# Performance work log

Hardware: AMD Instinct MI355X
Metric: run time of the kernel (lower is better)

The kernel has to match this reference:

```python
import jax, jax.numpy as jnp
import numpy as np

JIT = 1e-4
LOG2PI = float(np.log(2.0 * np.pi))
BETA = 1e5
LOC_RADIUS = 5.0


def gaspari_cohn(radius, D):
    i = np.arange(D)
    dist = np.minimum(np.abs(i[:, None] - i[None, :]), D - np.abs(i[:, None] - i[None, :])).astype(np.float64)
    z = dist / radius
    zs = np.maximum(z, 1e-12)
    g1 = 1.0 - 5.0 / 3 * z**2 + 5.0 / 8 * z**3 + 0.5 * z**4 - 0.25 * z**5
    g2 = 4.0 - 5.0 * z + 5.0 / 3 * z**2 + 5.0 / 8 * z**3 - 0.5 * z**4 + 1.0 / 12 * z**5 - 2.0 / (3.0 * zs)
    return np.where(z < 1.0, g1, np.where(z < 2.0, g2, 0.0)).astype(np.float32)


def sq_dist(x, z):
    # x: [..., n, d], z: [..., m, d] (broadcastable)
    x2 = jnp.sum(x * x, -1)[..., :, None]
    z2 = jnp.sum(z * z, -1)[..., None, :]
    d2 = x2 + z2 - 2.0 * jnp.matmul(x, jnp.swapaxes(z, -1, -2))
    return jnp.maximum(d2, 0.0)


def setup_inputs():
    key = jax.random.key(0)
    ks = jax.random.split(key, 12)
    D, dy, M, N, B, T = 32, 32, 128, 128, 8, 48
    ips = jax.random.normal(ks[0], (D, M, D), dtype=jnp.float32)
    H = jnp.eye(dy, D, dtype=jnp.float32)
    lengthscale = jnp.full((D,), 2.0, dtype=jnp.float32)
    outputscale = jnp.ones((D,), dtype=jnp.float32)
    q_mu = 0.1 * jax.random.normal(ks[1], (D, M), dtype=jnp.float32)
    q_L = jnp.tril(0.02 * jax.random.normal(ks[2], (D, M, M), dtype=jnp.float32), -1) + 0.1 * jnp.eye(M, dtype=jnp.float32)[None]
    q_noise = jnp.full((D,), 0.05**2, dtype=jnp.float32)
    r_noise = jnp.full((dy,), 0.1**2, dtype=jnp.float32)
    x0 = jax.random.normal(ks[3], (N, D, B, D), dtype=jnp.float32)
    y = 0.5 * jax.random.normal(ks[4], (B, T, dy), dtype=jnp.float32)
    eps_u = jax.random.normal(ks[5], (N, D, M), dtype=jnp.float32)
    eps_f = jax.random.normal(ks[6], (T, N, D, B), dtype=jnp.float32)
    eps_q = jax.random.normal(ks[7], (T, B, N, D), dtype=jnp.float32)
    eps_r = jax.random.normal(ks[8], (T, B, N, dy), dtype=jnp.float32)
    return {"ips": ips, "H": H, "lengthscale": lengthscale, "outputscale": outputscale,
            "q_mu": q_mu, "q_L": q_L, "q_noise": q_noise, "r_noise": r_noise,
            "x0": x0, "y": y, "eps_u": eps_u, "eps_f": eps_f, "eps_q": eps_q, "eps_r": eps_r}


def _forward(ips, H, lengthscale, outputscale, q_mu, q_L, q_noise, r_noise, x0, y, eps_u, eps_f, eps_q, eps_r):
    N, D, B, _ = x0.shape
    M = ips.shape[1]
    dy = y.shape[-1]
    taper = jnp.asarray(gaspari_cohn(LOC_RADIUS, D))
    ls = lengthscale[:, None, None]
    osc = outputscale[:, None, None]
    zs = ips / ls  # [D, M, D]
    Kzz = osc * jnp.exp(-0.5 * sq_dist(zs, zs)) + JIT * jnp.eye(M, dtype=x0.dtype)  # [D,M,M]
    # U ~ q(u): consistent sampling of inducing outputs per ensemble member
    U = q_mu[None] + jnp.einsum('dmk,ndk->ndm', q_L, eps_u)                 # [N,D,M]
    A = jnp.linalg.solve(Kzz[None], U[..., None])[..., 0]                    # Kzz^{-1} u, [N,D,M]
    # KL(q(u) || N(0, Kzz)) summed over tasks
    Lzz = jnp.linalg.cholesky(Kzz)
    Sq = q_L @ jnp.swapaxes(q_L, -1, -2)
    trace = jnp.sum(jnp.diagonal(jnp.linalg.solve(Kzz, Sq), axis1=-2, axis2=-1))
    mah = jnp.sum(q_mu * jnp.linalg.solve(Kzz, q_mu[..., None])[..., 0])
    logdetK = 2.0 * jnp.sum(jnp.log(jnp.diagonal(Lzz, axis1=-2, axis2=-1)))
    logdetS = 2.0 * jnp.sum(jnp.log(jnp.abs(jnp.diagonal(q_L, axis1=-2, axis2=-1))))
    kl = 0.5 * (trace + mah - D * M + logdetK - logdetS)

    q_sd = jnp.sqrt(q_noise)
    r_sd = jnp.sqrt(r_noise)
    R = jnp.diag(r_noise)
    Ht = H.T
    eyeB = jnp.eye(B, dtype=x0.dtype)

    def step(carry, inp):
        x_prev, ll = carry
        y_t, ef, eq, er = inp
        # ---- GP prediction (conditioned on sampled U) ----
        xq = x_prev / lengthscale[None, :, None, None]                       # [N,D,B,D]
        Kxz = outputscale[None, :, None, None] * jnp.exp(-0.5 * sq_dist(xq, zs[None]))  # [N,D,B,M]
        Kxx = outputscale[None, :, None, None] * jnp.exp(-0.5 * sq_dist(xq, xq))        # [N,D,B,B]
        mean = jnp.einsum('ndbm,ndm->ndb', Kxz, A)
        V = jnp.linalg.solve(Kzz[None], jnp.swapaxes(Kxz, -1, -2))           # [N,D,M,B]
        cov = Kxx - jnp.matmul(Kxz, V) + JIT * eyeB
        Lc = jnp.linalg.cholesky(cov)
        f = mean + jnp.einsum('ndbc,ndc->ndb', Lc, ef)                       # rsample, [N,D,B]
        X = jnp.transpose(f, (2, 0, 1))                                      # [B,N,D]
        X = X + eq * q_sd                                                    # + chol(Q) noise
        Xm = jnp.mean(X, axis=-2, keepdims=True)                             # [B,1,D]
        Xc = X - Xm
        P = taper * (jnp.swapaxes(Xc, -1, -2) @ Xc) / (N - 1)                # localized cov [B,D,D]
        # ---- EnKF update ----
        S = H @ P @ Ht + R                                                   # [B,dy,dy]
        Ls = jnp.linalg.cholesky(S)
        resid = y_t - (Xm @ Ht)[:, 0]                                        # [B,dy]
        alpha = jnp.linalg.solve(S, resid[..., None])[..., 0]
        logdetS_t = 2.0 * jnp.sum(jnp.log(jnp.diagonal(Ls, axis1=-2, axis2=-1)), axis=-1)
        ll_t = -0.5 * jnp.sum(dy * LOG2PI + logdetS_t + jnp.sum(resid * alpha, -1))
        PHt = P @ Ht
        K = jnp.swapaxes(jnp.linalg.solve(S, jnp.swapaxes(PHt, -1, -2)), -1, -2)  # [B,D,dy]
        y_pert = y_t[:, None, :] + er * r_sd
        X_post = X + (y_pert - X @ Ht) @ jnp.swapaxes(K, -1, -2)
        Xm_post = jnp.mean(X_post, axis=-2)                                  # [B,D]
        P_post = P - K @ (H @ P)
        x_next = jnp.broadcast_to(Xm_post[None, None], (N, D, B, D))         # ensemble reset to post. mean
        return (x_next, ll + ll_t), (Xm_post, jnp.diagonal(P_post, axis1=-2, axis2=-1))

    ys = jnp.swapaxes(y, 0, 1)  # [T,B,dy]
    (x_final, ll), (fm, fv) = jax.lax.scan(step, (x0, jnp.asarray(0.0, x0.dtype)), (ys, eps_f, eps_q, eps_r))
    filtered_mean = jnp.swapaxes(fm, 0, 1)  # [B,T,D]
    filtered_var = jnp.swapaxes(fv, 0, 1)   # [B,T,D]
    elbo = ll - kl / BETA
    return elbo, x_final, filtered_mean, filtered_var


def reference(ips, H, lengthscale, outputscale, q_mu, q_L, q_noise, r_noise, x0, y, eps_u, eps_f, eps_q, eps_r):
    return _forward(ips, H, lengthscale, outputscale, q_mu, q_L, q_noise, r_noise, x0, y, eps_u, eps_f, eps_q, eps_r)
```

## Files before the change

### kernel.cpp

```cpp
#include <hip/hip_runtime.h>

#define JITF 1e-4f
#define LOG2PIF 1.8378770664093454f

#define WZSM   0
#define WZS2   131072
#define WKINV  135168
#define WA     659456
#define WU     1183744
#define WXW    1708032
#define WXM    1740800
#define WLLB   1741056
#define WKLD   1741088
#define WCNT   1741248
#define OFM 1048577
#define OFV 1060865

__device__ __forceinline__ float dot4f(const float4 a, const float4 b) {
  return fmaf(a.x, b.x, fmaf(a.y, b.y, fmaf(a.z, b.z, a.w * b.w)));
}
__device__ __forceinline__ float4 f4_fma(const float4 a, const float s, const float4 c) {
  return make_float4(fmaf(a.x,s,c.x), fmaf(a.y,s,c.y), fmaf(a.z,s,c.z), fmaf(a.w,s,c.w));
}
__device__ __forceinline__ float4 f4_axpby(const float a, const float4 x, const float b, const float4 y) {
  return make_float4(fmaf(a,x.x,b*y.x), fmaf(a,x.y,b*y.y), fmaf(a,x.z,b*y.z), fmaf(a,x.w,b*y.w));
}
__device__ __forceinline__ float aloadf(const float* p) {
  return __hip_atomic_load((float*)p, __ATOMIC_RELAXED, __HIP_MEMORY_SCOPE_AGENT);
}
__device__ __forceinline__ void astoref(float* p, float v) {
  __hip_atomic_store(p, v, __ATOMIC_RELAXED, __HIP_MEMORY_SCOPE_AGENT);
}
__device__ __forceinline__ unsigned long long aloadu(const unsigned long long* p) {
  return __hip_atomic_load((unsigned long long*)p, __ATOMIC_RELAXED, __HIP_MEMORY_SCOPE_AGENT);
}
__device__ __forceinline__ void pollge(const int* p, int target) {
  while (__hip_atomic_load((int*)p, __ATOMIC_RELAXED, __HIP_MEMORY_SCOPE_AGENT) < target)
    __builtin_amdgcn_s_sleep(1);
}
__device__ __forceinline__ void gsignal(int* p, int val, int tid) {
  __syncthreads();
  if (tid == 0) __hip_atomic_store(p, val, __ATOMIC_RELEASE, __HIP_MEMORY_SCOPE_AGENT);
}

__global__ __launch_bounds__(512) void k_sweep(
    const float* __restrict__ ips, const float* __restrict__ ls, const float* __restrict__ osc,
    const float* __restrict__ qL, const float* __restrict__ qmu,
    float* __restrict__ zsMg, float* __restrict__ zs2g,
    float* __restrict__ Kinvg, float* __restrict__ kld, int* cnt)
{
  __shared__ float sm[22792];
  float* cur   = sm;
  float* zsM   = sm + 16896;
  float* rowP0 = sm + 21504;
  float* rowP1 = sm + 21636;
  float* colP0 = sm + 21768;
  float* colP1 = sm + 21896;
  float* qms   = sm + 22024;
  float* zs2   = sm + 22152;
  float* red   = sm + 22280;
  float4* cur4 = (float4*)cur;
  const float4* zsM4 = (const float4*)zsM;
  float4* rowP04 = (float4*)rowP0;
  float4* rowP14 = (float4*)rowP1;
  const int d = blockIdx.x, tid = threadIdx.x;
  const float invl = 1.0f / ls[d], oscd = osc[d];

  if (blockIdx.x == 0) { for (int l = tid; l < 640; l += 512) cnt[l] = 0; }

  for (int l = tid; l < 4096; l += 512) {
    int m = l >> 5, k = l & 31;
    zsM[m*36+k] = ips[(d*128+m)*32+k] * invl;
  }
  if (tid < 128) qms[tid] = qmu[d*128+tid];
  __syncthreads();
  if (tid < 128) {
    float s = 0.f;
#pragma unroll
    for (int kq = 0; kq < 8; kq++) { float4 v = zsM4[tid*9+kq]; s += dot4f(v, v); }
    zs2[tid] = s; zs2g[d*128+tid] = s;
  }
  for (int l = tid; l < 4096; l += 512) zsMg[d*4096+l] = zsM[(l>>5)*36 + (l&31)];
  __syncthreads();

  const int i = tid >> 2, q = tid & 3;
  {
    float4 zr[8];
#pragma unroll
    for (int kq = 0; kq < 8; kq++) zr[kq] = zsM4[i*9+kq];
    float z2i = zs2[i];
    for (int jj = 0; jj < 32; jj++) {
      int j = q*32 + jj;
      float dot = 0.f;
#pragma unroll
      for (int kq = 0; kq < 8; kq++) dot += dot4f(zr[kq], zsM4[j*9+kq]);
      float d2 = fmaxf(z2i + zs2[j] - 2.f*dot, 0.f);
      cur[i*132+j] = oscd * expf(-0.5f*d2) + (i == j ? JITF : 0.f);
    }
  }
  __syncthreads();

  float llog = 0.f;
#pragma unroll 1
  for (int kb = 0; kb < 64; kb++) {
    const int k0 = 2*kb, k1 = k0+1;
    if (tid < 33) rowP04[tid] = cur4[k0*33 + tid];
    else if (tid < 66) rowP14[tid-33] = cur4[k1*33 + (tid-33)];
    else if (tid < 194) colP0[tid-66] = cur[(tid-66)*132 + k0];
    else if (tid < 322) colP1[tid-194] = cur[(tid-194)*132 + k1];
    __syncthreads();
    const float a  = rowP0[k0];
    const float bb = rowP0[k1];
    const float c  = rowP1[k1];
    const float det = fmaf(a, c, -bb*bb);
    const float idet = 1.0f/det;
    if (tid == 0) llog += logf(det);
    const float ci0 = colP0[i], ci1 = colP1[i];
    const float w0 = (ci0*c - ci1*bb)*idet;
    const float w1 = (ci1*a - ci0*bb)*idet;
    const bool isk0 = (i == k0), isk1 = (i == k1);
    const int jqp = k0 >> 2;
    const int c0 = k0 & 3;
#pragma unroll
    for (int jj = 0; jj < 8; jj++) {
      int jq = q*8 + jj;
      float4 r0 = rowP04[jq];
      float4 r1 = rowP14[jq];
      float4 nv;
      if (isk0)      nv = f4_axpby(c*idet, r0, -bb*idet, r1);
      else if (isk1) nv = f4_axpby(-bb*idet, r0, a*idet, r1);
      else {
        nv = cur4[i*33+jq];
        nv = f4_fma(r0, -w0, nv);
        nv = f4_fma(r1, -w1, nv);
      }
      if (jq == jqp) {
        float pv0, pv1;
        if (isk0)      { pv0 = -c*idet;  pv1 =  bb*idet; }
        else if (isk1) { pv0 =  bb*idet; pv1 = -a*idet;  }
        else           { pv0 =  w0;      pv1 =  w1;      }
        if (c0 == 0) { nv.x = pv0; nv.y = pv1; }
        else         { nv.z = pv0; nv.w = pv1; }
      }
      cur4[i*33+jq] = nv;
    }
    __syncthreads();
  }
  for (int e = tid; e < 16384; e += 512) { int ii = e>>7, jj = e&127; cur[ii*132+jj] = -cur[ii*132+jj]; }
  __syncthreads();
  for (int l = tid; l < 4096; l += 512) ((float4*)(Kinvg + d*16384))[l] = cur4[(l>>5)*33 + (l&31)];

  if (tid == 0) kld[d] = 0.5f * llog;
  red[tid] = (tid < 128) ? logf(fabsf(qL[(d*128+tid)*128+tid])) : 0.f;
  __syncthreads();
  for (int s = 256; s > 0; s >>= 1) { if (tid < s) red[tid] += red[tid+s]; __syncthreads(); }
  if (tid == 0) kld[96+d] = red[0];
  __syncthreads();
  {
    float macc = 0.f;
    for (int e = tid; e < 16384; e += 512) {
      int ii = e >> 7, jj = e & 127;
      macc = fmaf(cur[ii*132+jj], qms[ii]*qms[jj], macc);
    }
    red[tid] = macc;
    __syncthreads();
    for (int s = 256; s > 0; s >>= 1) { if (tid < s) red[tid] += red[tid+s]; __syncthreads(); }
    if (tid == 0) kld[64+d] = red[0];
    __syncthreads();
  }
  {
    float tacc = 0.f;
    for (int e = tid; e < 16384; e += 512) {
      int ii = e >> 7, k2 = e & 127;
      if (k2 <= ii) {
        float w = 0.f;
        for (int m = k2; m < 128; m++) w = fmaf(cur[ii*132+m], qL[(d*128+m)*128+k2], w);
        tacc = fmaf(w, qL[(d*128+ii)*128+k2], tacc);
      }
    }
    red[tid] = tacc;
    __syncthreads();
    for (int s = 256; s > 0; s >>= 1) { if (tid < s) red[tid] += red[tid+s]; __syncthreads(); }
    if (tid == 0) kld[32+d] = red[0];
  }
}

__global__ __launch_bounds__(128) void k_U(
    const float* __restrict__ qL, const float* __restrict__ qmu, const float* __restrict__ eu,
    float* __restrict__ U)
{
  __shared__ float qLs[128][129];
  __shared__ float eus[128];
  const int d = blockIdx.x >> 2, nc = blockIdx.x & 3, tid = threadIdx.x;
  for (int l = tid; l < 16384; l += 128) qLs[l >> 7][l & 127] = qL[d * 16384 + l];
  __syncthreads();
  const float qm = qmu[d * 128 + tid];
  for (int nn = 0; nn < 32; nn++) {
    int n = nc * 32 + nn;
    eus[tid] = eu[(n * 32 + d) * 128 + tid];
    __syncthreads();
    int kmax = tid + 1;
    int k4 = kmax & ~3;
    float s0 = qm, s1 = 0.f, s2 = 0.f, s3 = 0.f;
    int k = 0;
    for (; k < k4; k += 4) {
      s0 = fmaf(qLs[tid][k], eus[k], s0);
      s1 = fmaf(qLs[tid][k + 1], eus[k + 1], s1);
      s2 = fmaf(qLs[tid][k + 2], eus[k + 2], s2);
      s3 = fmaf(qLs[tid][k + 3], eus[k + 3], s3);
    }
    for (; k < kmax; k++) s0 = fmaf(qLs[tid][k], eus[k], s0);
    U[(n * 32 + d) * 128 + tid] = (s0 + s1) + (s2 + s3);
    __syncthreads();
  }
}

__global__ __launch_bounds__(256) void k_A2(
    const float* __restrict__ Kinv, const float* __restrict__ U, float* __restrict__ A)
{
  __shared__ float Kis[128][129];
  __shared__ float Us[32][129];
  const int d = blockIdx.x >> 2, nc = blockIdx.x & 3, tid = threadIdx.x;
  const int n0 = nc * 32;
  for (int l = tid; l < 16384; l += 256) Kis[l >> 7][l & 127] = Kinv[d * 16384 + l];
  for (int l = tid; l < 4096; l += 256) Us[l >> 7][l & 127] = U[((n0 + (l >> 7)) * 32 + d) * 128 + (l & 127)];
  __syncthreads();
  for (int e = tid; e < 4096; e += 256) {
    int nl = e >> 7, m = e & 127;
    float s0 = 0.f, s1 = 0.f, s2 = 0.f, s3 = 0.f;
    for (int k = 0; k < 128; k += 4) {
      s0 = fmaf(Kis[m][k], Us[nl][k], s0);
      s1 = fmaf(Kis[m][k + 1], Us[nl][k + 1], s1);
      s2 = fmaf(Kis[m][k + 2], Us[nl][k + 2], s2);
      s3 = fmaf(Kis[m][k + 3], Us[nl][k + 3], s3);
    }
    A[((n0 + nl) * 32 + d) * 128 + m] = (s0 + s1) + (s2 + s3);
  }
}

__global__ __launch_bounds__(128) void k_t0gp(
    const float* __restrict__ x0, const float* __restrict__ ls, const float* __restrict__ osc,
    const float* __restrict__ qn, const float* __restrict__ zsMg, const float* __restrict__ zs2g,
    const float* __restrict__ Kinv, const float* __restrict__ A,
    const float* __restrict__ ef, const float* __restrict__ eq, float* __restrict__ Xw)
{
  __shared__ float xqs[8*36];
  __shared__ float xq2s[8];
  __shared__ float Kxzs[8*132];
  __shared__ float T1s[8*132];
  __shared__ float covs[8][9];
  __shared__ float Lc[8][9];
  __shared__ float Arow[132];
  const float4* xqs4  = (const float4*)xqs;
  const float4* Kxzs4 = (const float4*)Kxzs;
  const float4* T1s4  = (const float4*)T1s;
  const float4* Arow4 = (const float4*)Arow;
  const int n = blockIdx.x >> 5, d = blockIdx.x & 31, tid = threadIdx.x;
  const float invl = 1.0f / ls[d], oscd = osc[d];

  float4 zr[8];
  {
    const float4* zrow = (const float4*)(zsMg + d*4096 + tid*32);
#pragma unroll
    for (int kq = 0; kq < 8; kq++) zr[kq] = zrow[kq];
  }
  const float z2m = zs2g[d*128 + tid];
  for (int l = tid; l < 256; l += 128) {
    int b = l >> 5, k = l & 31;
    xqs[b*36+k] = x0[((n*32+d)*8 + b)*32 + k] * invl;
  }
  Arow[tid] = A[(n*32+d)*128 + tid];
  __syncthreads();
  if (tid < 8) {
    float s = 0.f;
#pragma unroll
    for (int kq = 0; kq < 8; kq++) { float4 v = xqs4[tid*9+kq]; s += dot4f(v, v); }
    xq2s[tid] = s;
  }
  __syncthreads();
  {
#pragma unroll
    for (int b = 0; b < 8; b++) {
      float dot = 0.f;
#pragma unroll
      for (int kq = 0; kq < 8; kq++) dot += dot4f(zr[kq], xqs4[b*9+kq]);
      Kxzs[b*132+tid] = oscd * expf(-0.5f * fmaxf(xq2s[b] + z2m - 2.f*dot, 0.f));
    }
  }
  __syncthreads();
  {
    float a[8] = {0.f,0.f,0.f,0.f,0.f,0.f,0.f,0.f};
    const float* kp = Kinv + d*16384 + tid;
    for (int mq = 0; mq < 32; mq++) {
      float kv0 = kp[(4*mq+0)*128];
      float kv1 = kp[(4*mq+1)*128];
      float kv2 = kp[(4*mq+2)*128];
      float kv3 = kp[(4*mq+3)*128];
#pragma unroll
      for (int b = 0; b < 8; b++) {
        float4 kx = Kxzs4[b*33+mq];
        a[b] = fmaf(kx.x, kv0, fmaf(kx.y, kv1, fmaf(kx.z, kv2, fmaf(kx.w, kv3, a[b]))));
      }
    }
#pragma unroll
    for (int b = 0; b < 8; b++) T1s[b*132+tid] = a[b];
  }
  __syncthreads();
  if (tid < 64) {
    int b = tid >> 3, c = tid & 7;
    float sc = 0.f, dt = 0.f;
#pragma unroll
    for (int mq = 0; mq < 32; mq++) sc += dot4f(T1s4[b*33+mq], Kxzs4[c*33+mq]);
#pragma unroll
    for (int kq = 0; kq < 8; kq++) dt += dot4f(xqs4[b*9+kq], xqs4[c*9+kq]);
    float kxx = oscd * expf(-0.5f * fmaxf(xq2s[b] + xq2s[c] - 2.f*dt, 0.f));
    covs[b][c] = kxx - sc + (b == c ? JITF : 0.f);
  }
  __syncthreads();
  if (tid == 0) {
    for (int a = 0; a < 8; a++) {
      float s = covs[a][a];
      for (int k = 0; k < a; k++) s -= Lc[a][k]*Lc[a][k];
      float la = sqrtf(s);
      Lc[a][a] = la;
      for (int i2 = a+1; i2 < 8; i2++) {
        float s2 = covs[i2][a];
        for (int k = 0; k < a; k++) s2 -= Lc[i2][k]*Lc[a][k];
        Lc[i2][a] = s2 / la;
      }
    }
  }
  __syncthreads();
  if (tid < 8) {
    int b = tid;
    float mv = 0.f;
#pragma unroll
    for (int mq = 0; mq < 32; mq++) mv += dot4f(Kxzs4[b*33+mq], Arow4[mq]);
    float f = mv;
#pragma unroll
    for (int c = 0; c < 8; c++) if (c <= b) f = fmaf(Lc[b][c], ef[(n*32+d)*8 + c], f);
    float X = f + eq[(b*128+n)*32 + d] * sqrtf(qn[d]);
    Xw[(d*8+b)*128 + n] = X;
  }
}

__global__ __launch_bounds__(1024) void k_scan(
    const float* __restrict__ ls, const float* __restrict__ osc,
    const float* __restrict__ qn, const float* __restrict__ rn,
    const float* __restrict__ y,
    const float* __restrict__ ef, const float* __restrict__ eq, const float* __restrict__ er,
    const float* __restrict__ zsMg, const float* __restrict__ zs2g,
    const float* __restrict__ Kinvg, const float* __restrict__ Ag,
    float* Xw, float* xm, float* llb, const float* __restrict__ kld,
    float* out, int* cnt)
{
  __shared__ float sm[36704];
  const int blk = blockIdx.x, tid = threadIdx.x;

  if (blk < 32) {
    const int d = blk;
    float* KinvS = sm;
    float* AT    = sm + 16512;
    float* KxzS  = sm + 33024;
    float* T1S   = sm + 34080;
    float* xqS   = sm + 35136;
    float* efS   = sm + 35424;
    float* covS  = sm + 36576;
    const float invl = 1.0f/ls[d], oscd = osc[d], qsd = sqrtf(qn[d]);
    const float4* KxzS4 = (const float4*)KxzS;
    const float4* T1S4  = (const float4*)T1S;
    const float4* xqS4  = (const float4*)xqS;
    const unsigned long long* xm_u = (const unsigned long long*)xm;

    for (int l = tid; l < 16384; l += 1024)
      KinvS[(l>>7)*129 + (l&127)] = Kinvg[d*16384 + l];
    for (int l = tid; l < 16384; l += 1024) {
      int n = l >> 7, m = l & 127;
      AT[m*129 + n] = Ag[(n*32 + d)*128 + m];
    }

    const int bb = tid >> 7, mn = tid & 127;
    float4 zr[8];
    {
      const float4* zrow = (const float4*)(zsMg + d*4096 + mn*32);
#pragma unroll
      for (int kq = 0; kq < 8; kq++) zr[kq] = zrow[kq];
    }
    const float z2m = zs2g[d*128 + mn];
    __syncthreads();

    for (int t = 1; t < 48; t++) {
      const float v_ef = ef[((t*128 + (tid>>3))*32 + d)*8 + (tid&7)];
      const float v_eq = eq[((t*8+bb)*128 + mn)*32 + d];

      if (tid < 8) pollge(cnt + (32+tid)*16, t);
      __syncthreads();
      if (tid < 128) {
        unsigned long long u = aloadu(xm_u + tid);
        float2 f = __builtin_bit_cast(float2, u);
        int b2 = tid >> 4, k2 = (tid & 15)*2;
        xqS[b2*36 + k2]     = f.x * invl;
        xqS[b2*36 + k2 + 1] = f.y * invl;
      }
      efS[(tid>>3)*9 + (tid&7)] = v_ef;
      __syncthreads();
      {
        float dot = 0.f, sq = 0.f;
#pragma unroll
        for (int kq = 0; kq < 8; kq++) {
          float4 x4 = xqS4[bb*9+kq];
          dot += dot4f(zr[kq], x4);
          sq  += dot4f(x4, x4);
        }
        KxzS[bb*132+mn] = oscd * expf(-0.5f * fmaxf(sq + z2m - 2.f*dot, 0.f));
      }
      __syncthreads();
      float mv;
      {
        float t1a = 0.f, t1b = 0.f, ma = 0.f, mb2 = 0.f;
#pragma unroll 8
        for (int mm = 0; mm < 128; mm += 2) {
          float kx0 = KxzS[bb*132+mm], kx1 = KxzS[bb*132+mm+1];
          t1a = fmaf(kx0, KinvS[mm*129+mn],     t1a);
          t1b = fmaf(kx1, KinvS[(mm+1)*129+mn], t1b);
          ma  = fmaf(kx0, AT[mm*129+mn],        ma);
          mb2 = fmaf(kx1, AT[(mm+1)*129+mn],    mb2);
        }
        T1S[bb*132+mn] = t1a + t1b;
        mv = ma + mb2;
      }
      __syncthreads();
      if (tid < 64) {
        int b = tid >> 3, c = tid & 7;
        float sc = 0.f, dt = 0.f, sqb = 0.f, sqc = 0.f;
#pragma unroll
        for (int mq = 0; mq < 32; mq++) sc += dot4f(T1S4[b*33+mq], KxzS4[c*33+mq]);
#pragma unroll
        for (int kq = 0; kq < 8; kq++) {
          float4 xb = xqS4[b*9+kq], xc = xqS4[c*9+kq];
          dt += dot4f(xb, xc); sqb += dot4f(xb, xb); sqc += dot4f(xc, xc);
        }
        float kxx = oscd*expf(-0.5f*fmaxf(sqb + sqc - 2.f*dt, 0.f));
        covS[b*9+c] = kxx - sc + (b==c ? JITF : 0.f);
      }
      __syncthreads();
      {
        float Lc[8][8];
        float f = mv;
#pragma unroll
        for (int a = 0; a < 8; a++) {
          float s = covS[a*9+a];
#pragma unroll
          for (int k = 0; k < 8; k++) if (k < a) s -= Lc[a][k]*Lc[a][k];
          float la = sqrtf(s);
          Lc[a][a] = la;
          if (a == bb) f = fmaf(la, efS[mn*9+a], f);
          float ila = 1.0f / la;
#pragma unroll
          for (int i2 = 0; i2 < 8; i2++) if (i2 > a) {
            float s2 = covS[i2*9+a];
#pragma unroll
            for (int k = 0; k < 8; k++) if (k < a) s2 -= Lc[i2][k]*Lc[a][k];
            float lv = s2 * ila;
            Lc[i2][a] = lv;
            if (i2 == bb) f = fmaf(lv, efS[mn*9+a], f);
          }
        }
        f = fmaf(v_eq, qsd, f);
        astoref(Xw + (d*8+bb)*128 + mn, f);
      }
      gsignal(cnt + d*16, t, tid);
    }
    if (tid < 8) pollge(cnt + (32+tid)*16, 48);
    __syncthreads();
  } else {
    const int b = blk - 32;
    float* XN     = sm;
    float* Ps     = sm + 4224;
    float* Sinvs  = sm + 5376;
    float* taperS = sm + 6432;
    float* mersS  = sm + 7456;
    float* rowP   = sm + 8992;
    float* colP   = sm + 9136;
    float* detS   = sm + 9280;
    float* XmsS   = sm + 9296;
    float* residS = sm + 9328;
    float* miS    = sm + 9360;
    float* rsdS   = sm + 9392;
    float* rnS    = sm + 9424;
    const float4* er4 = (const float4*)er;
    const unsigned long long* Xw_u = (const unsigned long long*)Xw;

    if (tid < 1024) {
      int ii = tid >> 5, jj = tid & 31;
      int ad = ii - jj; if (ad < 0) ad = -ad;
      int dist = (ad < 32 - ad) ? ad : (32 - ad);
      double z = (double)dist / 5.0;
      double z2 = z*z, z3 = z2*z, z4 = z3*z, z5 = z4*z;
      double gval;
      if (z < 1.0) gval = 1.0 - (5.0/3.0)*z2 + (5.0/8.0)*z3 + 0.5*z4 - 0.25*z5;
      else if (z < 2.0) gval = 4.0 - 5.0*z + (5.0/3.0)*z2 + (5.0/8.0)*z3 - 0.5*z4 + (1.0/12.0)*z5 - 2.0/(3.0*z);
      else gval = 0.0;
      taperS[tid] = (float)gval;
    }
    if (tid < 32) { rnS[tid] = rn[tid]; rsdS[tid] = sqrtf(rn[tid]); }
    if (tid < 384) {
      int tt = tid >> 3, jq = tid & 7;
      float sx = 0.f, sy = 0.f, sz = 0.f, sw = 0.f;
      for (int n = 0; n < 128; n++) {
        float4 e = er4[((tt*8+b)*128+n)*8 + jq];
        sx += e.x; sy += e.y; sz += e.z; sw += e.w;
      }
      int o = tt*32 + jq*4;
      mersS[o]   = sx*(1.f/128.f);
      mersS[o+1] = sy*(1.f/128.f);
      mersS[o+2] = sz*(1.f/128.f);
      mersS[o+3] = sw*(1.f/128.f);
    }
    __syncthreads();

    float llacc = 0.f;
    const int i = tid >> 5, j = tid & 31;
    for (int t = 0; t < 48; t++) {
      float yv = 0.f;
      if (tid < 32) yv = y[(b*48+t)*32 + tid];
      if (t > 0) { if (tid < 32) pollge(cnt + tid*16, t); }
      __syncthreads();
      {
        unsigned long long u0 = aloadu(Xw_u + (i*8+b)*64 + j);
        unsigned long long u1 = aloadu(Xw_u + (i*8+b)*64 + j + 32);
        float2 f0 = __builtin_bit_cast(float2, u0);
        float2 f1 = __builtin_bit_cast(float2, u1);
        float s4 = (f0.x+f0.y)+(f1.x+f1.y);
#pragma unroll
        for (int mk = 1; mk <= 16; mk <<= 1) s4 += __shfl_xor(s4, mk, 64);
        float mu = s4 * (1.f/128.f);
        if (j == 0) XmsS[i] = mu;
        XN[(2*j)*33+i]    = f0.x - mu;
        XN[(2*j+1)*33+i]  = f0.y - mu;
        XN[(2*j+64)*33+i] = f1.x - mu;
        XN[(2*j+65)*33+i] = f1.y - mu;
      }
      __syncthreads();
      float val;
      {
        float a0 = 0.f, a1 = 0.f;
#pragma unroll 4
        for (int n = 0; n < 128; n += 2) {
          a0 = fmaf(XN[n*33+i],     XN[n*33+j],     a0);
          a1 = fmaf(XN[(n+1)*33+i], XN[(n+1)*33+j], a1);
        }
        float pv = taperS[i*32+j] * (a0+a1) * (1.f/127.f);
        Ps[i*36+j] = pv;
        val = pv + ((i==j) ? rnS[i] : 0.f);
      }
#pragma unroll 1
      for (int kb = 0; kb < 16; kb++) {
        int k0 = kb*2, k1 = k0+1, par = (kb&1)*72;
        if (i == k0) rowP[par + j]      = val;
        if (i == k1) rowP[par + 36 + j] = val;
        if (j == k0) colP[par + i]      = val;
        if (j == k1) colP[par + 36 + i] = val;
        __syncthreads();
        float a  = rowP[par + k0];
        float bb = rowP[par + k1];
        float c  = rowP[par + 36 + k1];
        float det = fmaf(a, c, -bb*bb);
        float idet = 1.0f/det;
        float ci0 = colP[par + i], ci1 = colP[par + 36 + i];
        float r0j = rowP[par + j], r1j = rowP[par + 36 + j];
        float w0 = (ci0*c - ci1*bb)*idet;
        float w1 = (ci1*a - ci0*bb)*idet;
        float v0 = (c*r0j - bb*r1j)*idet;
        float v1 = (a*r1j - bb*r0j)*idet;
        float nv = val - w0*r0j - w1*r1j;
        if (i == k0) nv = v0;
        if (i == k1) nv = v1;
        if (j == k0) nv = w0;
        if (j == k1) nv = w1;
        if (i == k0 && j == k0) nv = -c*idet;
        if (i == k0 && j == k1) nv =  bb*idet;
        if (i == k1 && j == k0) nv =  bb*idet;
        if (i == k1 && j == k1) nv = -a*idet;
        val = nv;
        if (tid == 0) detS[kb] = det;
      }
      Sinvs[i*33+j] = -val;
      if (tid < 32) {
        float rs = yv - XmsS[tid];
        residS[tid] = rs;
        miS[tid] = fmaf(mersS[t*32+tid], rsdS[tid], rs);
      }
      __syncthreads();
      if (tid < 32) {
        float bt = 0.f;
#pragma unroll
        for (int k = 0; k < 32; k++) bt = fmaf(Sinvs[tid*33+k], miS[k], bt);
        float xmp = XmsS[tid] + miS[tid] - rnS[tid]*bt;
        out[OFM + (b*48+t)*32 + tid] = xmp;
        out[OFV + (b*48+t)*32 + tid] = rnS[tid] - rnS[tid]*rnS[tid]*Sinvs[tid*33+tid];
        astoref(xm + b*32 + tid, xmp);
      } else if (tid < 64) {
        int ii = tid - 32;
        float al = 0.f;
#pragma unroll
        for (int k = 0; k < 32; k++) al = fmaf(Sinvs[ii*33+k], residS[k], al);
        float contrib = al * residS[ii] + ((ii < 16) ? logf(detS[ii]) : 0.f);
#pragma unroll
        for (int mk = 1; mk <= 16; mk <<= 1) contrib += __shfl_xor(contrib, mk, 64);
        if (ii == 0) {
          llacc += -0.5f*(32.f*LOG2PIF + contrib);
          if (t == 47) astoref(llb + b, llacc);
        }
      }
      gsignal(cnt + (32+b)*16, t+1, tid);
    }
    if (tid < 8) pollge(cnt + (32+tid)*16, 48);
    __syncthreads();
  }

  if (tid < 128) {
    unsigned long long u = aloadu((const unsigned long long*)xm + tid);
    float2 f = __builtin_bit_cast(float2, u);
    sm[2*tid] = f.x; sm[2*tid+1] = f.y;
  }
  __syncthreads();
  for (int v = blk*1024 + tid; v < 1048576; v += 40960)
    out[1 + v] = sm[v & 255];
  if (blk == 32 && tid == 0) {
    double ll = 0.0;
    for (int i2 = 0; i2 < 8; i2++) ll += (double)aloadf(llb + i2);
    double ldK = 0.0, tr = 0.0, mah = 0.0, ldS = 0.0;
    for (int d2 = 0; d2 < 32; d2++) {
      ldK += (double)kld[d2];
      tr  += (double)kld[32+d2];
      mah += (double)kld[64+d2];
      ldS += (double)kld[96+d2];
    }
    double klv = 0.5*(tr + mah - 4096.0 + 2.0*ldK - 2.0*ldS);
    out[0] = (float)(ll - klv/100000.0);
  }
}

extern "C" void kernel_launch(void* const* d_in, const int* in_sizes, int n_in,
                              void* d_out, int out_size, void* d_ws, size_t ws_size,
                              hipStream_t stream) {
  const float* ips = (const float*)d_in[0];
  const float* ls  = (const float*)d_in[2];
  const float* osc = (const float*)d_in[3];
  const float* qmu = (const float*)d_in[4];
  const float* qL  = (const float*)d_in[5];
  const float* qn  = (const float*)d_in[6];
  const float* rn  = (const float*)d_in[7];
  const float* x0  = (const float*)d_in[8];
  const float* y   = (const float*)d_in[9];
  const float* eu  = (const float*)d_in[10];
  const float* ef  = (const float*)d_in[11];
  const float* eq  = (const float*)d_in[12];
  const float* er  = (const float*)d_in[13];
  float* out = (float*)d_out;
  float* ws  = (float*)d_ws;

  float* w_zsm  = ws + WZSM;
  float* w_zs2  = ws + WZS2;
  float* w_kinv = ws + WKINV;
  float* w_A    = ws + WA;
  float* w_U    = ws + WU;
  float* w_Xw   = ws + WXW;
  float* w_xm   = ws + WXM;
  float* w_llb  = ws + WLLB;
  float* w_kld  = ws + WKLD;
  int*   w_cnt  = (int*)(ws + WCNT);

  k_sweep<<<32, 512, 0, stream>>>(ips, ls, osc, qL, qmu, w_zsm, w_zs2, w_kinv, w_kld, w_cnt);
  k_U<<<128, 128, 0, stream>>>(qL, qmu, eu, w_U);
  k_A2<<<128, 256, 0, stream>>>(w_kinv, w_U, w_A);
  k_t0gp<<<4096, 128, 0, stream>>>(x0, ls, osc, qn, w_zsm, w_zs2, w_kinv, w_A, ef, eq, w_Xw);
  void* args[] = { (void*)&ls, (void*)&osc, (void*)&qn, (void*)&rn, (void*)&y,
                   (void*)&ef, (void*)&eq, (void*)&er, (void*)&w_zsm, (void*)&w_zs2,
                   (void*)&w_kinv, (void*)&w_A, (void*)&w_Xw, (void*)&w_xm, (void*)&w_llb,
                   (void*)&w_kld, (void*)&out, (void*)&w_cnt };
  hipLaunchCooperativeKernel((void*)k_scan, dim3(40), dim3(1024), args, 0, stream);
}
```

Measured before the change: 1.917 ms.

## Register-block GP mean/T1 matvec, symmetric covariance, and 4x4-block Gauss-Jordan inverse

In the per-dimension blocks, the Kxz·Kinv and Kxz·A products are now computed by 256 threads. Each thread holds float4 rows of Kinv/A and reuses them across 4 batch rows. Results are written to shared memory instead of each of 1024 threads doing a scalar dot. In the filter blocks, the ensemble covariance uses only the 528 upper-triangle entries via float4 dot products and a mean correction instead of explicit centering. The in-place inversion now pivots on 4x4 blocks, which halves the number of barrier-separated steps. The changes aim to cut LDS traffic and sync count on the serial scan path, at the cost of fewer active threads, more registers, and possible cancellation in the uncentered covariance.

```diff
diff --git a/kernel.cpp b/kernel.cpp
--- a/kernel.cpp
+++ b/kernel.cpp
@@ -354,29 +354,32 @@
     float* Xw, float* xm, float* llb, const float* __restrict__ kld,
     float* out, int* cnt)
 {
-  __shared__ float sm[36704];
+  __shared__ float sm[38740];
   const int blk = blockIdx.x, tid = threadIdx.x;
 
   if (blk < 32) {
     const int d = blk;
     float* KinvS = sm;
-    float* AT    = sm + 16512;
-    float* KxzS  = sm + 33024;
-    float* T1S   = sm + 34080;
-    float* xqS   = sm + 35136;
-    float* efS   = sm + 35424;
-    float* covS  = sm + 36576;
+    float* AS    = sm + 16896;
+    float* KxzS  = sm + 33792;
+    float* T1S   = sm + 34848;
+    float* MeanS = sm + 35904;
+    float* xqS   = sm + 36960;
+    float* efS   = sm + 37248;
+    float* covS  = sm + 38400;
     const float invl = 1.0f/ls[d], oscd = osc[d], qsd = sqrtf(qn[d]);
-    const float4* KxzS4 = (const float4*)KxzS;
-    const float4* T1S4  = (const float4*)T1S;
-    const float4* xqS4  = (const float4*)xqS;
+    const float4* KinvS4 = (const float4*)KinvS;
+    const float4* AS4    = (const float4*)AS;
+    const float4* KxzS4  = (const float4*)KxzS;
+    const float4* T1S4   = (const float4*)T1S;
+    const float4* xqS4   = (const float4*)xqS;
     const unsigned long long* xm_u = (const unsigned long long*)xm;
 
     for (int l = tid; l < 16384; l += 1024)
-      KinvS[(l>>7)*129 + (l&127)] = Kinvg[d*16384 + l];
+      KinvS[(l>>7)*132 + (l&127)] = Kinvg[d*16384 + l];
     for (int l = tid; l < 16384; l += 1024) {
       int n = l >> 7, m = l & 127;
-      AT[m*129 + n] = Ag[(n*32 + d)*128 + m];
+      AS[n*132 + m] = Ag[(n*32 + d)*128 + m];
     }
 
     const int bb = tid >> 7, mn = tid & 127;
@@ -415,19 +418,26 @@
         KxzS[bb*132+mn] = oscd * expf(-0.5f * fmaxf(sq + z2m - 2.f*dot, 0.f));
       }
       __syncthreads();
-      float mv;
-      {
-        float t1a = 0.f, t1b = 0.f, ma = 0.f, mb2 = 0.f;
+      if (tid < 256) {
+        const int bq = tid >> 7, mq = tid & 127;
+        float t1a[4] = {0.f,0.f,0.f,0.f};
+        float mea[4] = {0.f,0.f,0.f,0.f};
 #pragma unroll 8
-        for (int mm = 0; mm < 128; mm += 2) {
-          float kx0 = KxzS[bb*132+mm], kx1 = KxzS[bb*132+mm+1];
-          t1a = fmaf(kx0, KinvS[mm*129+mn],     t1a);
-          t1b = fmaf(kx1, KinvS[(mm+1)*129+mn], t1b);
-          ma  = fmaf(kx0, AT[mm*129+mn],        ma);
-          mb2 = fmaf(kx1, AT[(mm+1)*129+mn],    mb2);
+        for (int mmq = 0; mmq < 32; mmq++) {
+          float4 kv = KinvS4[mq*33 + mmq];
+          float4 av = AS4[mq*33 + mmq];
+#pragma unroll
+          for (int c = 0; c < 4; c++) {
+            float4 kx = KxzS4[(bq + 2*c)*33 + mmq];
+            t1a[c] += dot4f(kx, kv);
+            mea[c] += dot4f(kx, av);
+          }
         }
-        T1S[bb*132+mn] = t1a + t1b;
-        mv = ma + mb2;
+#pragma unroll
+        for (int c = 0; c < 4; c++) {
+          T1S[(bq + 2*c)*132 + mq]   = t1a[c];
+          MeanS[(bq + 2*c)*132 + mq] = mea[c];
+        }
       }
       __syncthreads();
       if (tid < 64) {
@@ -446,7 +456,7 @@
       __syncthreads();
       {
         float Lc[8][8];
-        float f = mv;
+        float f = MeanS[bb*132 + mn];
 #pragma unroll
         for (int a = 0; a < 8; a++) {
           float s = covS[a*9+a];
@@ -475,19 +485,20 @@
     __syncthreads();
   } else {
     const int b = blk - 32;
-    float* XN     = sm;
+    float* XT     = sm;
     float* Ps     = sm + 4224;
     float* Sinvs  = sm + 5376;
     float* taperS = sm + 6432;
     float* mersS  = sm + 7456;
     float* rowP   = sm + 8992;
-    float* colP   = sm + 9136;
-    float* detS   = sm + 9280;
-    float* XmsS   = sm + 9296;
-    float* residS = sm + 9328;
-    float* miS    = sm + 9360;
-    float* rsdS   = sm + 9392;
-    float* rnS    = sm + 9424;
+    float* colP   = sm + 9280;
+    float* detS   = sm + 9568;
+    float* XmsS   = sm + 9576;
+    float* residS = sm + 9608;
+    float* miS    = sm + 9640;
+    float* rsdS   = sm + 9672;
+    float* rnS    = sm + 9704;
+    const float4* XT4 = (const float4*)XT;
     const float4* er4 = (const float4*)er;
     const unsigned long long* Xw_u = (const unsigned long long*)Xw;
 
@@ -517,6 +528,12 @@
       mersS[o+2] = sz*(1.f/128.f);
       mersS[o+3] = sw*(1.f/128.f);
     }
+    int ti = -1, tj = -1;
+    if (tid < 528) {
+      int row = 0, rem = tid;
+      while (rem >= 32 - row) { rem -= 32 - row; row++; }
+      ti = row; tj = row + rem;
+    }
     __syncthreads();
 
     float llacc = 0.f;
@@ -534,56 +551,85 @@
         float s4 = (f0.x+f0.y)+(f1.x+f1.y);
 #pragma unroll
         for (int mk = 1; mk <= 16; mk <<= 1) s4 += __shfl_xor(s4, mk, 64);
-        float mu = s4 * (1.f/128.f);
-        if (j == 0) XmsS[i] = mu;
-        XN[(2*j)*33+i]    = f0.x - mu;
-        XN[(2*j+1)*33+i]  = f0.y - mu;
-        XN[(2*j+64)*33+i] = f1.x - mu;
-        XN[(2*j+65)*33+i] = f1.y - mu;
-      }
-      __syncthreads();
-      float val;
-      {
-        float a0 = 0.f, a1 = 0.f;
-#pragma unroll 4
-        for (int n = 0; n < 128; n += 2) {
-          a0 = fmaf(XN[n*33+i],     XN[n*33+j],     a0);
-          a1 = fmaf(XN[(n+1)*33+i], XN[(n+1)*33+j], a1);
+        if (j == 0) XmsS[i] = s4 * (1.f/128.f);
+        XT[i*132 + 2*j]      = f0.x;
+        XT[i*132 + 2*j + 1]  = f0.y;
+        XT[i*132 + 2*j + 64] = f1.x;
+        XT[i*132 + 2*j + 65] = f1.y;
+      }
+      __syncthreads();
+      if (tid < 528) {
+        float g = 0.f;
+#pragma unroll 8
+        for (int nq = 0; nq < 32; nq++) g += dot4f(XT4[ti*33+nq], XT4[tj*33+nq]);
+        float pv = taperS[ti*32+tj] * (g - 128.f*XmsS[ti]*XmsS[tj]) * (1.f/127.f);
+        Ps[ti*36+tj] = pv;
+        Ps[tj*36+ti] = pv;
+      }
+      __syncthreads();
+      float val = Ps[i*36+j] + ((i==j) ? rnS[i] : 0.f);
+#pragma unroll 1
+      for (int kb = 0; kb < 8; kb++) {
+        const int k0 = kb*4;
+        float* rowPb = rowP + (kb&1)*144;
+        float* colPb = colP + (kb&1)*144;
+        if (i >= k0 && i < k0+4) rowPb[(i-k0)*36 + j] = val;
+        if (j >= k0 && j < k0+4) colPb[(j-k0)*36 + i] = val;
+        __syncthreads();
+        float p00 = rowPb[0*36+k0+0], p01 = rowPb[0*36+k0+1], p02 = rowPb[0*36+k0+2], p03 = rowPb[0*36+k0+3];
+        float p11 = rowPb[1*36+k0+1], p12 = rowPb[1*36+k0+2], p13 = rowPb[1*36+k0+3];
+        float p22 = rowPb[2*36+k0+2], p23 = rowPb[2*36+k0+3], p33 = rowPb[3*36+k0+3];
+        float deta = fmaf(p00, p11, -p01*p01);
+        float ia = 1.0f/deta;
+        float ai00 = p11*ia, ai01 = -p01*ia, ai11 = p00*ia;
+        float m00 = ai00*p02 + ai01*p12;
+        float m01 = ai00*p03 + ai01*p13;
+        float m10 = ai01*p02 + ai11*p12;
+        float m11 = ai01*p03 + ai11*p13;
+        float s00 = p22 - (p02*m00 + p12*m10);
+        float s01 = p23 - (p02*m01 + p12*m11);
+        float s11 = p33 - (p03*m01 + p13*m11);
+        float dets = fmaf(s00, s11, -s01*s01);
+        float is = 1.0f/dets;
+        float si00 = s11*is, si01 = -s01*is, si11 = s00*is;
+        float n00 = m00*si00 + m01*si01;
+        float n01 = m00*si01 + m01*si11;
+        float n10 = m10*si00 + m11*si01;
+        float n11 = m10*si01 + m11*si11;
+        float q00 = ai00 + n00*m00 + n01*m01;
+        float q01 = ai01 + n00*m10 + n01*m11;
+        float q11 = ai11 + n10*m10 + n11*m11;
+        const float PI[4][4] = {
+          {  q00,  q01, -n00, -n01 },
+          {  q01,  q11, -n10, -n11 },
+          { -n00, -n10, si00, si01 },
+          { -n01, -n11, si01, si11 }
+        };
+        if (tid == 0) detS[kb] = deta * dets;
+        float cI[4], rJ[4];
+#pragma unroll
+        for (int a = 0; a < 4; a++) { cI[a] = colPb[a*36 + i]; rJ[a] = rowPb[a*36 + j]; }
+        float w[4];
+#pragma unroll
+        for (int bq = 0; bq < 4; bq++)
+          w[bq] = cI[0]*PI[0][bq] + cI[1]*PI[1][bq] + cI[2]*PI[2][bq] + cI[3]*PI[3][bq];
+        float interior = val - (w[0]*rJ[0] + w[1]*rJ[1] + w[2]*rJ[2] + w[3]*rJ[3]);
+        const int r = i - k0, c = j - k0;
+        const bool ip = (r >= 0 && r < 4), jp = (c >= 0 && c < 4);
+        float pr[4], pc[4];
+#pragma unroll
+        for (int bq = 0; bq < 4; bq++) {
+          pr[bq] = (r==0) ? PI[0][bq] : (r==1) ? PI[1][bq] : (r==2) ? PI[2][bq] : PI[3][bq];
+          pc[bq] = (c==0) ? PI[bq][0] : (c==1) ? PI[bq][1] : (c==2) ? PI[bq][2] : PI[bq][3];
         }
-        float pv = taperS[i*32+j] * (a0+a1) * (1.f/127.f);
-        Ps[i*36+j] = pv;
-        val = pv + ((i==j) ? rnS[i] : 0.f);
-      }
-#pragma unroll 1
-      for (int kb = 0; kb < 16; kb++) {
-        int k0 = kb*2, k1 = k0+1, par = (kb&1)*72;
-        if (i == k0) rowP[par + j]      = val;
-        if (i == k1) rowP[par + 36 + j] = val;
-        if (j == k0) colP[par + i]      = val;
-        if (j == k1) colP[par + 36 + i] = val;
-        __syncthreads();
-        float a  = rowP[par + k0];
-        float bb = rowP[par + k1];
-        float c  = rowP[par + 36 + k1];
-        float det = fmaf(a, c, -bb*bb);
-        float idet = 1.0f/det;
-        float ci0 = colP[par + i], ci1 = colP[par + 36 + i];
-        float r0j = rowP[par + j], r1j = rowP[par + 36 + j];
-        float w0 = (ci0*c - ci1*bb)*idet;
-        float w1 = (ci1*a - ci0*bb)*idet;
-        float v0 = (c*r0j - bb*r1j)*idet;
-        float v1 = (a*r1j - bb*r0j)*idet;
-        float nv = val - w0*r0j - w1*r1j;
-        if (i == k0) nv = v0;
-        if (i == k1) nv = v1;
-        if (j == k0) nv = w0;
-        if (j == k1) nv = w1;
-        if (i == k0 && j == k0) nv = -c*idet;
-        if (i == k0 && j == k1) nv =  bb*idet;
-        if (i == k1 && j == k0) nv =  bb*idet;
-        if (i == k1 && j == k1) nv = -a*idet;
+        float rowv = pr[0]*rJ[0] + pr[1]*rJ[1] + pr[2]*rJ[2] + pr[3]*rJ[3];
+        float colv = cI[0]*pc[0] + cI[1]*pc[1] + cI[2]*pc[2] + cI[3]*pc[3];
+        float prc  = (c==0) ? pr[0] : (c==1) ? pr[1] : (c==2) ? pr[2] : pr[3];
+        float nv = interior;
+        if (ip) nv = rowv;
+        if (jp) nv = colv;
+        if (ip && jp) nv = -prc;
         val = nv;
-        if (tid == 0) detS[kb] = det;
       }
       Sinvs[i*33+j] = -val;
       if (tid < 32) {
@@ -605,7 +651,7 @@
         float al = 0.f;
 #pragma unroll
         for (int k = 0; k < 32; k++) al = fmaf(Sinvs[ii*33+k], residS[k], al);
-        float contrib = al * residS[ii] + ((ii < 16) ? logf(detS[ii]) : 0.f);
+        float contrib = al * residS[ii] + ((ii < 8) ? logf(detS[ii]) : 0.f);
 #pragma unroll
         for (int mk = 1; mk <= 16; mk <<= 1) contrib += __shfl_xor(contrib, mk, 64);
         if (ii == 0) {
```

New measurement: 2.171 ms. 1.13x slower.

## Widen sweep kernel to 1024 threads, cache qL in LDS, fuse U and A kernels

Applied to the files above, without the earlier changes.

The Gauss-Jordan sweep kernel now runs 1024 threads per block, with 8 threads per row instead of 4, so each step's elimination work is spread across more lanes. The KL trace term now reads qL from a shared-memory copy rather than from global memory. The separate U and A kernels are merged into one, which keeps U in LDS and removes a launch plus a global round trip. In exchange, shared memory per block grows substantially and the sweep pays a wider barrier on each of its 64 steps.

```diff
diff --git a/kernel.cpp b/kernel.cpp
--- a/kernel.cpp
+++ b/kernel.cpp
@@ -7,7 +7,6 @@
 #define WZS2   131072
 #define WKINV  135168
 #define WA     659456
-#define WU     1183744
 #define WXW    1708032
 #define WXM    1740800
 #define WLLB   1741056
@@ -43,22 +42,23 @@
   if (tid == 0) __hip_atomic_store(p, val, __ATOMIC_RELEASE, __HIP_MEMORY_SCOPE_AGENT);
 }
 
-__global__ __launch_bounds__(512) void k_sweep(
+__global__ __launch_bounds__(1024) void k_sweep(
     const float* __restrict__ ips, const float* __restrict__ ls, const float* __restrict__ osc,
     const float* __restrict__ qL, const float* __restrict__ qmu,
     float* __restrict__ zsMg, float* __restrict__ zs2g,
     float* __restrict__ Kinvg, float* __restrict__ kld, int* cnt)
 {
-  __shared__ float sm[22792];
+  __shared__ float sm[40200];
   float* cur   = sm;
-  float* zsM   = sm + 16896;
-  float* rowP0 = sm + 21504;
-  float* rowP1 = sm + 21636;
-  float* colP0 = sm + 21768;
-  float* colP1 = sm + 21896;
-  float* qms   = sm + 22024;
-  float* zs2   = sm + 22152;
-  float* red   = sm + 22280;
+  float* qLs   = sm + 16896;
+  float* zsM   = sm + 33792;
+  float* rowP0 = sm + 38400;
+  float* rowP1 = sm + 38532;
+  float* colP0 = sm + 38664;
+  float* colP1 = sm + 38792;
+  float* qms   = sm + 38920;
+  float* zs2   = sm + 39048;
+  float* red   = sm + 39176;
   float4* cur4 = (float4*)cur;
   const float4* zsM4 = (const float4*)zsM;
   float4* rowP04 = (float4*)rowP0;
@@ -66,12 +66,14 @@
   const int d = blockIdx.x, tid = threadIdx.x;
   const float invl = 1.0f / ls[d], oscd = osc[d];
 
-  if (blockIdx.x == 0) { for (int l = tid; l < 640; l += 512) cnt[l] = 0; }
-
-  for (int l = tid; l < 4096; l += 512) {
+  if (blockIdx.x == 0) { for (int l = tid; l < 640; l += 1024) cnt[l] = 0; }
+
+  for (int l = tid; l < 4096; l += 1024) {
     int m = l >> 5, k = l & 31;
     zsM[m*36+k] = ips[(d*128+m)*32+k] * invl;
   }
+  for (int l = tid; l < 16384; l += 1024)
+    qLs[(l>>7)*132 + (l&127)] = qL[d*16384 + l];
   if (tid < 128) qms[tid] = qmu[d*128+tid];
   __syncthreads();
   if (tid < 128) {
@@ -80,17 +82,17 @@
     for (int kq = 0; kq < 8; kq++) { float4 v = zsM4[tid*9+kq]; s += dot4f(v, v); }
     zs2[tid] = s; zs2g[d*128+tid] = s;
   }
-  for (int l = tid; l < 4096; l += 512) zsMg[d*4096+l] = zsM[(l>>5)*36 + (l&31)];
-  __syncthreads();
-
-  const int i = tid >> 2, q = tid & 3;
+  for (int l = tid; l < 4096; l += 1024) zsMg[d*4096+l] = zsM[(l>>5)*36 + (l&31)];
+  __syncthreads();
+
+  const int i = tid >> 3, q = tid & 7;
   {
     float4 zr[8];
 #pragma unroll
     for (int kq = 0; kq < 8; kq++) zr[kq] = zsM4[i*9+kq];
     float z2i = zs2[i];
-    for (int jj = 0; jj < 32; jj++) {
-      int j = q*32 + jj;
+    for (int jj = 0; jj < 16; jj++) {
+      int j = q*16 + jj;
       float dot = 0.f;
 #pragma unroll
       for (int kq = 0; kq < 8; kq++) dot += dot4f(zr[kq], zsM4[j*9+kq]);
@@ -121,9 +123,7 @@
     const bool isk0 = (i == k0), isk1 = (i == k1);
     const int jqp = k0 >> 2;
     const int c0 = k0 & 3;
-#pragma unroll
-    for (int jj = 0; jj < 8; jj++) {
-      int jq = q*8 + jj;
+    auto body = [&](int jq) {
       float4 r0 = rowP04[jq];
       float4 r1 = rowP14[jq];
       float4 nv;
@@ -143,98 +143,90 @@
         else         { nv.z = pv0; nv.w = pv1; }
       }
       cur4[i*33+jq] = nv;
-    }
-    __syncthreads();
-  }
-  for (int e = tid; e < 16384; e += 512) { int ii = e>>7, jj = e&127; cur[ii*132+jj] = -cur[ii*132+jj]; }
-  __syncthreads();
-  for (int l = tid; l < 4096; l += 512) ((float4*)(Kinvg + d*16384))[l] = cur4[(l>>5)*33 + (l&31)];
+    };
+#pragma unroll
+    for (int jj = 0; jj < 4; jj++) body(q*4 + jj);
+    if (q == 7) body(32);
+    __syncthreads();
+  }
+  for (int e = tid; e < 16384; e += 1024) { int ii = e>>7, jj = e&127; cur[ii*132+jj] = -cur[ii*132+jj]; }
+  __syncthreads();
+  for (int l = tid; l < 4096; l += 1024) ((float4*)(Kinvg + d*16384))[l] = cur4[(l>>5)*33 + (l&31)];
 
   if (tid == 0) kld[d] = 0.5f * llog;
-  red[tid] = (tid < 128) ? logf(fabsf(qL[(d*128+tid)*128+tid])) : 0.f;
-  __syncthreads();
-  for (int s = 256; s > 0; s >>= 1) { if (tid < s) red[tid] += red[tid+s]; __syncthreads(); }
+  red[tid] = (tid < 128) ? logf(fabsf(qLs[tid*132+tid])) : 0.f;
+  __syncthreads();
+  for (int s = 512; s > 0; s >>= 1) { if (tid < s) red[tid] += red[tid+s]; __syncthreads(); }
   if (tid == 0) kld[96+d] = red[0];
   __syncthreads();
   {
     float macc = 0.f;
-    for (int e = tid; e < 16384; e += 512) {
+    for (int e = tid; e < 16384; e += 1024) {
       int ii = e >> 7, jj = e & 127;
       macc = fmaf(cur[ii*132+jj], qms[ii]*qms[jj], macc);
     }
     red[tid] = macc;
     __syncthreads();
-    for (int s = 256; s > 0; s >>= 1) { if (tid < s) red[tid] += red[tid+s]; __syncthreads(); }
+    for (int s = 512; s > 0; s >>= 1) { if (tid < s) red[tid] += red[tid+s]; __syncthreads(); }
     if (tid == 0) kld[64+d] = red[0];
     __syncthreads();
   }
   {
     float tacc = 0.f;
-    for (int e = tid; e < 16384; e += 512) {
+    for (int e = tid; e < 16384; e += 1024) {
       int ii = e >> 7, k2 = e & 127;
       if (k2 <= ii) {
         float w = 0.f;
-        for (int m = k2; m < 128; m++) w = fmaf(cur[ii*132+m], qL[(d*128+m)*128+k2], w);
-        tacc = fmaf(w, qL[(d*128+ii)*128+k2], tacc);
+        for (int m = k2; m < 128; m++) w = fmaf(cur[ii*132+m], qLs[m*132+k2], w);
+        tacc = fmaf(w, qLs[ii*132+k2], tacc);
       }
     }
     red[tid] = tacc;
     __syncthreads();
-    for (int s = 256; s > 0; s >>= 1) { if (tid < s) red[tid] += red[tid+s]; __syncthreads(); }
+    for (int s = 512; s > 0; s >>= 1) { if (tid < s) red[tid] += red[tid+s]; __syncthreads(); }
     if (tid == 0) kld[32+d] = red[0];
   }
 }
 
-__global__ __launch_bounds__(128) void k_U(
+__global__ __launch_bounds__(256) void k_UA(
     const float* __restrict__ qL, const float* __restrict__ qmu, const float* __restrict__ eu,
-    float* __restrict__ U)
+    const float* __restrict__ Kinv, float* __restrict__ A)
 {
-  __shared__ float qLs[128][129];
-  __shared__ float eus[128];
-  const int d = blockIdx.x >> 2, nc = blockIdx.x & 3, tid = threadIdx.x;
-  for (int l = tid; l < 16384; l += 128) qLs[l >> 7][l & 127] = qL[d * 16384 + l];
-  __syncthreads();
-  const float qm = qmu[d * 128 + tid];
-  for (int nn = 0; nn < 32; nn++) {
-    int n = nc * 32 + nn;
-    eus[tid] = eu[(n * 32 + d) * 128 + tid];
-    __syncthreads();
-    int kmax = tid + 1;
-    int k4 = kmax & ~3;
-    float s0 = qm, s1 = 0.f, s2 = 0.f, s3 = 0.f;
-    int k = 0;
-    for (; k < k4; k += 4) {
-      s0 = fmaf(qLs[tid][k], eus[k], s0);
-      s1 = fmaf(qLs[tid][k + 1], eus[k + 1], s1);
-      s2 = fmaf(qLs[tid][k + 2], eus[k + 2], s2);
-      s3 = fmaf(qLs[tid][k + 3], eus[k + 3], s3);
-    }
-    for (; k < kmax; k++) s0 = fmaf(qLs[tid][k], eus[k], s0);
-    U[(n * 32 + d) * 128 + tid] = (s0 + s1) + (s2 + s3);
-    __syncthreads();
-  }
-}
-
-__global__ __launch_bounds__(256) void k_A2(
-    const float* __restrict__ Kinv, const float* __restrict__ U, float* __restrict__ A)
-{
-  __shared__ float Kis[128][129];
-  __shared__ float Us[32][129];
+  __shared__ float big[16512];
+  __shared__ float Us[4128];
+  __shared__ float eus[4128];
   const int d = blockIdx.x >> 2, nc = blockIdx.x & 3, tid = threadIdx.x;
   const int n0 = nc * 32;
-  for (int l = tid; l < 16384; l += 256) Kis[l >> 7][l & 127] = Kinv[d * 16384 + l];
-  for (int l = tid; l < 4096; l += 256) Us[l >> 7][l & 127] = U[((n0 + (l >> 7)) * 32 + d) * 128 + (l & 127)];
+  for (int l = tid; l < 16384; l += 256) big[(l>>7)*129 + (l&127)] = qL[d*16384 + l];
+  for (int l = tid; l < 4096; l += 256)
+    eus[(l>>7)*129 + (l&127)] = eu[((n0 + (l>>7))*32 + d)*128 + (l&127)];
+  __syncthreads();
+  for (int e = tid; e < 4096; e += 256) {
+    int nl = e >> 7, m = e & 127;
+    float s0 = qmu[d*128 + m], s1 = 0.f, s2 = 0.f, s3 = 0.f;
+    int kmax = m + 1, k4 = kmax & ~3, k = 0;
+    for (; k < k4; k += 4) {
+      s0 = fmaf(big[m*129+k],   eus[nl*129+k],   s0);
+      s1 = fmaf(big[m*129+k+1], eus[nl*129+k+1], s1);
+      s2 = fmaf(big[m*129+k+2], eus[nl*129+k+2], s2);
+      s3 = fmaf(big[m*129+k+3], eus[nl*129+k+3], s3);
+    }
+    for (; k < kmax; k++) s0 = fmaf(big[m*129+k], eus[nl*129+k], s0);
+    Us[nl*129+m] = (s0+s1)+(s2+s3);
+  }
+  __syncthreads();
+  for (int l = tid; l < 16384; l += 256) big[(l>>7)*129 + (l&127)] = Kinv[d*16384 + l];
   __syncthreads();
   for (int e = tid; e < 4096; e += 256) {
     int nl = e >> 7, m = e & 127;
     float s0 = 0.f, s1 = 0.f, s2 = 0.f, s3 = 0.f;
     for (int k = 0; k < 128; k += 4) {
-      s0 = fmaf(Kis[m][k], Us[nl][k], s0);
-      s1 = fmaf(Kis[m][k + 1], Us[nl][k + 1], s1);
-      s2 = fmaf(Kis[m][k + 2], Us[nl][k + 2], s2);
-      s3 = fmaf(Kis[m][k + 3], Us[nl][k + 3], s3);
-    }
-    A[((n0 + nl) * 32 + d) * 128 + m] = (s0 + s1) + (s2 + s3);
+      s0 = fmaf(big[m*129+k],   Us[nl*129+k],   s0);
+      s1 = fmaf(big[m*129+k+1], Us[nl*129+k+1], s1);
+      s2 = fmaf(big[m*129+k+2], Us[nl*129+k+2], s2);
+      s3 = fmaf(big[m*129+k+3], Us[nl*129+k+3], s3);
+    }
+    A[((n0+nl)*32 + d)*128 + m] = (s0+s1)+(s2+s3);
   }
 }
 
@@ -665,16 +657,14 @@
   float* w_zs2  = ws + WZS2;
   float* w_kinv = ws + WKINV;
   float* w_A    = ws + WA;
-  float* w_U    = ws + WU;
   float* w_Xw   = ws + WXW;
   float* w_xm   = ws + WXM;
   float* w_llb  = ws + WLLB;
   float* w_kld  = ws + WKLD;
   int*   w_cnt  = (int*)(ws + WCNT);
 
-  k_sweep<<<32, 512, 0, stream>>>(ips, ls, osc, qL, qmu, w_zsm, w_zs2, w_kinv, w_kld, w_cnt);
-  k_U<<<128, 128, 0, stream>>>(qL, qmu, eu, w_U);
-  k_A2<<<128, 256, 0, stream>>>(w_kinv, w_U, w_A);
+  k_sweep<<<32, 1024, 0, stream>>>(ips, ls, osc, qL, qmu, w_zsm, w_zs2, w_kinv, w_kld, w_cnt);
+  k_UA<<<128, 256, 0, stream>>>(qL, qmu, eu, w_kinv, w_A);
   k_t0gp<<<4096, 128, 0, stream>>>(x0, ls, osc, qn, w_zsm, w_zs2, w_kinv, w_A, ef, eq, w_Xw);
   void* args[] = { (void*)&ls, (void*)&osc, (void*)&qn, (void*)&rn, (void*)&y,
                    (void*)&ef, (void*)&eq, (void*)&er, (void*)&w_zsm, (void*)&w_zs2,
```

Result: faster. 1.625 ms (-15.2%).
